# Kernel tuning notes

Measured on AMD Instinct MI355X. Metric: run time of the kernel, lower is better.

Reference implementation:

```python
import jax, jax.numpy as jnp
import numpy as np

EMBED_DIM = 1024
NUM_HEADS = 16
HEAD_DIM = EMBED_DIM // NUM_HEADS
ROPE_BASE = 10000.0


def _rope_angles(seq_len, head_dim):
    inv_freq = 1.0 / (ROPE_BASE ** (jnp.arange(0, head_dim, 2, dtype=jnp.float32) / head_dim))  # [D/2]
    pos = jnp.arange(seq_len, dtype=jnp.float32)
    ang = pos[:, None] * inv_freq[None, :]  # [S, D/2]
    return jnp.cos(ang), jnp.sin(ang)


def _apply_rope(t, cos, sin):
    # t: [B, H, S, D]; rotate-half convention
    d2 = t.shape[-1] // 2
    t1, t2 = t[..., :d2], t[..., d2:]
    return jnp.concatenate([t1 * cos - t2 * sin, t2 * cos + t1 * sin], axis=-1)


def setup_inputs() -> dict:
    key = jax.random.key(0)
    ks = jax.random.split(key, 6)
    B, S, E = 1, 4096, EMBED_DIM
    x = jax.random.normal(ks[0], (B, S, E), dtype=jnp.float32)
    # causal mask: True means masked-out (upper triangle above diagonal)
    mask = jnp.triu(jnp.ones((S, S), dtype=bool), k=1)[None, None, :, :]
    scale = 0.02
    wqkv_w = jax.random.normal(ks[1], (E, 3 * E), dtype=jnp.float32) * scale
    wqkv_b = jax.random.normal(ks[2], (3 * E,), dtype=jnp.float32) * scale
    out_w = jax.random.normal(ks[3], (E, E), dtype=jnp.float32) * scale
    out_b = jax.random.normal(ks[4], (E,), dtype=jnp.float32) * scale
    return {"x": x, "mask": mask, "wqkv_w": wqkv_w, "wqkv_b": wqkv_b, "out_w": out_w, "out_b": out_b}


def reference(x, mask, wqkv_w, wqkv_b, out_w, out_b):
    B, S, E = x.shape
    H, D = NUM_HEADS, HEAD_DIM
    qkv = x @ wqkv_w + wqkv_b  # [B, S, 3E]
    q, k, v = jnp.split(qkv, 3, axis=-1)
    # [B, S, E] -> [B, H, S, D]
    q = q.reshape(B, S, H, D).transpose(0, 2, 1, 3)
    k = k.reshape(B, S, H, D).transpose(0, 2, 1, 3)
    v = v.reshape(B, S, H, D).transpose(0, 2, 1, 3)
    cos, sin = _rope_angles(S, D)  # [S, D/2]
    q = _apply_rope(q, cos, sin)
    k = _apply_rope(k, cos, sin)
    scores = jnp.einsum('bhqd,bhkd->bhqk', q, k) * (D ** -0.5)  # [B, H, S, S]
    scores = jnp.where(mask[:, :, -S:, :], -jnp.inf, scores)
    weights = jax.nn.softmax(scores, axis=-1)
    ctx = jnp.einsum('bhqk,bhkd->bhqd', weights, v)  # [B, H, S, D]
    ctx = ctx.transpose(0, 2, 1, 3).reshape(B, S, E)
    return ctx @ out_w + out_b
```

## Files before the change

kernel.cpp:

```cpp
#include <hip/hip_runtime.h>
#include <hip/hip_bf16.h>
#include <math.h>

#define S_LEN 4096
#define EMB   1024
#define E3    3072
#define NH    16
#define HD    64

#define SLOTS_PER_HEAD 52
#define NSLOTS         832

typedef unsigned short u16;
typedef short          bfrag __attribute__((ext_vector_type(8)));
typedef float          ffrag __attribute__((ext_vector_type(4)));
typedef unsigned short us8   __attribute__((ext_vector_type(8)));
typedef unsigned short us4   __attribute__((ext_vector_type(4)));

__device__ __forceinline__ u16 f2bf(float f) {
    union { float f; unsigned u; } v; v.f = f;
    unsigned r = v.u + 0x7fffu + ((v.u >> 16) & 1u);
    return (u16)(r >> 16);
}
__device__ __forceinline__ float bf2f(u16 b) {
    union { unsigned u; float f; } v; v.u = ((unsigned)b) << 16;
    return v.f;
}
__device__ __forceinline__ unsigned pack_bf16_trunc(float lo, float hi) {
    union { float f; unsigned u; } a, b; a.f = lo; b.f = hi;
    return __builtin_amdgcn_perm(b.u, a.u, 0x07060302u);
}
__device__ __forceinline__ void gld16(const void* g, void* l) {
    __builtin_amdgcn_global_load_lds(
        (const __attribute__((address_space(1))) unsigned int*)g,
        (__attribute__((address_space(3))) unsigned int*)l, 16, 0, 0);
}

__global__ __launch_bounds__(256)
void cast_bf16_kernel(const float* __restrict__ in, u16* __restrict__ out) {
    const size_t i = ((size_t)blockIdx.x * 256 + threadIdx.x) * 8;
    float4 a = *(const float4*)(in + i);
    float4 b = *(const float4*)(in + i + 4);
    us8 o;
    o[0]=f2bf(a.x); o[1]=f2bf(a.y); o[2]=f2bf(a.z); o[3]=f2bf(a.w);
    o[4]=f2bf(b.x); o[5]=f2bf(b.y); o[6]=f2bf(b.z); o[7]=f2bf(b.w);
    *(us8*)(out + i) = o;
}

__global__ __launch_bounds__(256)
void transpose_cast_kernel(const float* __restrict__ in, u16* __restrict__ out,
                           int R, int C) {
    __shared__ u16 T[64][72];
    const int r0 = blockIdx.x * 64, c0 = blockIdx.y * 64;
    const int t = threadIdx.x;
    const int rr = t >> 2, cc = (t & 3) * 16;

    const float* ip = in + (size_t)(r0 + rr) * C + c0 + cc;
    u16 tmp[16];
    #pragma unroll
    for (int i4 = 0; i4 < 4; i4++) {
        float4 v = ((const float4*)ip)[i4];
        tmp[4*i4+0]=f2bf(v.x); tmp[4*i4+1]=f2bf(v.y);
        tmp[4*i4+2]=f2bf(v.z); tmp[4*i4+3]=f2bf(v.w);
    }
    #pragma unroll
    for (int i8 = 0; i8 < 2; i8++) {
        us8 vv;
        #pragma unroll
        for (int j = 0; j < 8; j++) vv[j] = tmp[8*i8+j];
        *(us8*)&T[rr][cc + 8*i8] = vv;
    }
    __syncthreads();

    const int oc = t >> 2, orr = (t & 3) * 16;
    u16 ot[16];
    #pragma unroll
    for (int j = 0; j < 16; j++) ot[j] = T[orr + j][oc];
    u16* op = out + (size_t)(c0 + oc) * R + r0 + orr;
    #pragma unroll
    for (int i8 = 0; i8 < 2; i8++) {
        us8 vv;
        #pragma unroll
        for (int j = 0; j < 8; j++) vv[j] = ot[8*i8+j];
        *(us8*)(op + 8*i8) = vv;
    }
}

template <int OUT_BF16, int NT, int ROPE, int MINW>
__global__ __launch_bounds__(256, MINW)
void gemm_bt_kernel(const u16* __restrict__ A, const u16* __restrict__ Bt,
                    const float* __restrict__ bias, void* __restrict__ Cv,
                    u16* __restrict__ vtp, int M, int N, int K) {
    constexpr int BN = 32 * NT;
    constexpr int WS = 16 * NT;
    __shared__ u16 As[2][128][32];
    __shared__ u16 Bs[2][BN][32];

    const int tid = threadIdx.x;
    const int w = tid >> 6, L = tid & 63;
    const int col = L & 15, quad = L >> 4;
    const int wm = w & 1, wn = w >> 1;
    const int m0 = blockIdx.x * 128, n0 = blockIdx.y * BN;

    ffrag acc[4][NT];
    #pragma unroll
    for (int a = 0; a < 4; a++)
        #pragma unroll
        for (int b = 0; b < NT; b++)
            #pragma unroll
            for (int r = 0; r < 4; r++) acc[a][b][r] = 0.f;

    const int srow = L >> 2;
    const int schk = L & 3;

    #pragma unroll
    for (int t = 0; t < 2; t++) {
        const int rg = (2 * w + t) * 16;
        gld16(A + (size_t)(m0 + rg + srow) * K + schk * 8, &As[0][rg][0]);
    }
    #pragma unroll
    for (int t = 0; t < NT / 2; t++) {
        const int rg = (w * (NT / 2) + t) * 16;
        gld16(Bt + (size_t)(n0 + rg + srow) * K + schk * 8, &Bs[0][rg][0]);
    }
    __syncthreads();

    int buf = 0;
    for (int k0 = 0; k0 < K; k0 += 32, buf ^= 1) {
        if (k0 + 32 < K) {
            #pragma unroll
            for (int t = 0; t < 2; t++) {
                const int rg = (2 * w + t) * 16;
                gld16(A + (size_t)(m0 + rg + srow) * K + k0 + 32 + schk * 8,
                      &As[buf ^ 1][rg][0]);
            }
            #pragma unroll
            for (int t = 0; t < NT / 2; t++) {
                const int rg = (w * (NT / 2) + t) * 16;
                gld16(Bt + (size_t)(n0 + rg + srow) * K + k0 + 32 + schk * 8,
                      &Bs[buf ^ 1][rg][0]);
            }
        }

        bfrag af[4], bf[NT];
        #pragma unroll
        for (int mt = 0; mt < 4; mt++)
            af[mt] = *(const bfrag*)&As[buf][64 * wm + 16 * mt + col][8 * quad];
        #pragma unroll
        for (int nt = 0; nt < NT; nt++)
            bf[nt] = *(const bfrag*)&Bs[buf][WS * wn + 16 * nt + col][8 * quad];
        #pragma unroll
        for (int mt = 0; mt < 4; mt++)
            #pragma unroll
            for (int nt = 0; nt < NT; nt++)
                acc[mt][nt] = __builtin_amdgcn_mfma_f32_16x16x32_bf16(
                    af[mt], bf[nt], acc[mt][nt], 0, 0, 0);

        __syncthreads();
    }

    float bv[NT];
    #pragma unroll
    for (int nt = 0; nt < NT; nt++) bv[nt] = bias[n0 + WS * wn + 16 * nt + col];

    if (ROPE && n0 < 2 * EMB) {
        const float SCq = (n0 < EMB) ? 0.125f * 1.44269504088896f : 1.0f;
        const float C = 13.287712379549449f / 32.0f;
        float invf[2];
        invf[0] = exp2f(-(float)col * C);
        invf[1] = exp2f(-(float)(col + 16) * C);
        #pragma unroll
        for (int mt = 0; mt < 4; mt++) {
            #pragma unroll
            for (int r = 0; r < 4; r++) {
                const int mrow = m0 + 64 * wm + 16 * mt + 4 * quad + r;
                const float fs = (float)mrow;
                u16* cp = (u16*)Cv + (size_t)mrow * N + n0 + 64 * wn + col;
                #pragma unroll
                for (int pr = 0; pr < 2; pr++) {
                    float sn, cs;
                    sincosf(fs * invf[pr], &sn, &cs);
                    const float t1 = acc[mt][pr][r] + bv[pr];
                    const float t2 = acc[mt][pr + 2][r] + bv[pr + 2];
                    cp[16 * pr]      = f2bf((t1 * cs - t2 * sn) * SCq);
                    cp[16 * pr + 32] = f2bf((t2 * cs + t1 * sn) * SCq);
                }
            }
        }
    } else if (ROPE) {
        #pragma unroll
        for (int nt = 0; nt < NT; nt++) {
            const int dg = n0 - 2 * EMB + WS * wn + 16 * nt + col;
            #pragma unroll
            for (int mt = 0; mt < 4; mt++) {
                const int s0 = m0 + 64 * wm + 16 * mt + 4 * quad;
                us4 pk;
                #pragma unroll
                for (int r = 0; r < 4; r++) pk[r] = f2bf(acc[mt][nt][r] + bv[nt]);
                *(us4*)&vtp[(size_t)dg * S_LEN + s0] = pk;
            }
        }
    } else {
        #pragma unroll
        for (int mt = 0; mt < 4; mt++) {
            #pragma unroll
            for (int r = 0; r < 4; r++) {
                const int m = m0 + 64 * wm + 16 * mt + 4 * quad + r;
                #pragma unroll
                for (int nt = 0; nt < NT; nt++) {
                    const int n = n0 + WS * wn + 16 * nt + col;
                    const float val = acc[mt][nt][r] + bv[nt];
                    if (OUT_BF16) ((u16*)Cv)[(size_t)m * N + n] = f2bf(val);
                    else          ((float*)Cv)[(size_t)m * N + n] = val;
                }
            }
        }
    }
}

__global__ __launch_bounds__(256, 3)
void flash10_kernel(const u16* __restrict__ qkvb, const u16* __restrict__ vt,
                    u16* __restrict__ ctxb, u16* __restrict__ pO,
                    float* __restrict__ pL) {
    __shared__ u16 QP[4][32][64];
    __shared__ u16 Ks[2][64][64];
    __shared__ u16 Vs[2][64][64];

    const int id = blockIdx.x;
    const int x  = id & 7;
    const int tt = id >> 3;
    const int h  = x + 8 * (tt & 1);
    const int o  = tt >> 1;

    int qi, ch, nc;
    if (o < 30)      { qi = 31 - o / 3;        ch = o % 3;        nc = 3; }
    else if (o < 33) { qi = 10 - (o - 30);     ch = 0;            nc = 1; }
    else if (o < 55) { const int oo = o - 33;  qi = 21 - oo / 2;  ch = oo & 1; nc = 2; }
    else             { qi = 7 - (o - 55);      ch = 0;            nc = 1; }

    const int total = 2 * qi + 2;
    const int Lc    = (total + nc - 1) / nc;
    const int kt0   = ch * Lc;
    const int cnt   = min(Lc, total - kt0);
    const bool lastch = (kt0 + cnt == total);
    const int q0 = qi * 128;

    const int tid = threadIdx.x;
    const int w = tid >> 6, L = tid & 63;
    const int col = L & 15, quad = L >> 4;
    const int lr = L >> 3, lp = L & 7;
    const int lc = lp ^ lr;

    const bool domask = lastch;
    const int nwt = cnt - ((domask && w < 2) ? 1 : 0);

    const size_t kArow = (size_t)(16 * w + lr) * E3 + EMB + h * HD + lc * 8;
    const size_t vArow = ((size_t)h * HD + 16 * w + lr) * S_LEN + lc * 8;
    const size_t kt0off  = (size_t)kt0 * 64 * E3;
    const size_t vt0off  = (size_t)kt0 * 64;

    #pragma unroll
    for (int u = 0; u < 4; u++)
        gld16(qkvb + (size_t)(q0 + 32 * w + 8 * u + lr) * E3 + h * HD + lc * 8,
              &QP[w][8 * u][0]);
    #pragma unroll
    for (int u = 0; u < 2; u++) {
        gld16(qkvb + kArow + kt0off + (size_t)(8 * u) * E3,
              &Ks[0][16 * w + 8 * u][0]);
        gld16(vt + vArow + vt0off + (size_t)(8 * u) * S_LEN,
              &Vs[0][16 * w + 8 * u][0]);
    }
    __syncthreads();

    bfrag qf[2][2];
    #pragma unroll
    for (int i = 0; i < 2; i++)
        #pragma unroll
        for (int ks = 0; ks < 2; ks++)
            qf[i][ks] = *(const bfrag*)
                ((const char*)&QP[w][16 * i + col][0] +
                 16 * ((4 * ks + quad) ^ (col & 7)));

    bfrag ones;
    #pragma unroll
    for (int i = 0; i < 8; i++) ones[i] = (short)0x3F80;

    ffrag o_[4][2], ol[2];
    #pragma unroll
    for (int d4 = 0; d4 < 4; d4++)
        #pragma unroll
        for (int i = 0; i < 2; i++)
            #pragma unroll
            for (int r2 = 0; r2 < 4; r2++) o_[d4][i][r2] = 0.f;
    #pragma unroll
    for (int i = 0; i < 2; i++)
        #pragma unroll
        for (int r2 = 0; r2 < 4; r2++) ol[i][r2] = 0.f;

    #pragma unroll 1
    for (int t = 0; t < cnt; t++) {
        const int buf = t & 1;
        if (t + 1 < cnt) {
            const size_t ko = kArow + kt0off + (size_t)(t + 1) * 64 * E3;
            const size_t vo = vArow + vt0off + (size_t)(t + 1) * 64;
            #pragma unroll
            for (int u = 0; u < 2; u++) {
                gld16(qkvb + ko + (size_t)(8 * u) * E3,
                      &Ks[buf ^ 1][16 * w + 8 * u][0]);
                gld16(vt + vo + (size_t)(8 * u) * S_LEN,
                      &Vs[buf ^ 1][16 * w + 8 * u][0]);
            }
        }

        if (t < nwt) {
            ffrag st[4][2];
            #pragma unroll
            for (int t4 = 0; t4 < 4; t4++)
                #pragma unroll
                for (int i = 0; i < 2; i++)
                    #pragma unroll
                    for (int r2 = 0; r2 < 4; r2++) st[t4][i][r2] = 0.f;
            #pragma unroll
            for (int ks = 0; ks < 2; ks++) {
                bfrag kf[4];
                #pragma unroll
                for (int t4 = 0; t4 < 4; t4++)
                    kf[t4] = *(const bfrag*)
                        &Ks[buf][16 * t4 + col][(((4 * ks + quad) ^ (col & 7)) * 8)];
                #pragma unroll
                for (int t4 = 0; t4 < 4; t4++)
                    #pragma unroll
                    for (int i = 0; i < 2; i++)
                        st[t4][i] = __builtin_amdgcn_mfma_f32_16x16x32_bf16(
                            kf[t4], qf[i][ks], st[t4][i], 0, 0, 0);
            }

            if (domask && t == nwt - 1) {
                #pragma unroll
                for (int i = 0; i < 2; i++) {
                    const int qrel = 32 * (w & 1) + 16 * i + col;
                    #pragma unroll
                    for (int t4 = 0; t4 < 4; t4++) {
                        const int key0 = 16 * t4 + 4 * quad;
                        #pragma unroll
                        for (int r2 = 0; r2 < 4; r2++)
                            if (key0 + r2 > qrel) st[t4][i][r2] = -3.0e38f;
                    }
                }
            }

            #pragma unroll
            for (int i = 0; i < 2; i++) {
                const int prow = 16 * i + col;
                #pragma unroll
                for (int t4 = 0; t4 < 4; t4++) {
                    float pr[4];
                    #pragma unroll
                    for (int r2 = 0; r2 < 4; r2++) pr[r2] = exp2f(st[t4][i][r2]);
                    uint2 pk;
                    pk.x = pack_bf16_trunc(pr[0], pr[1]);
                    pk.y = pack_bf16_trunc(pr[2], pr[3]);
                    const int c2 = (2 * t4 + (quad >> 1)) ^ (col & 7);
                    *(uint2*)((char*)&QP[w][prow][0] + 16 * c2 + 8 * (quad & 1)) = pk;
                }
            }

            #pragma unroll
            for (int ks = 0; ks < 2; ks++) {
                bfrag vf[4];
                #pragma unroll
                for (int d4 = 0; d4 < 4; d4++)
                    vf[d4] = *(const bfrag*)
                        &Vs[buf][16 * d4 + col][(((4 * ks + quad) ^ (col & 7)) * 8)];
                bfrag pf[2];
                #pragma unroll
                for (int i = 0; i < 2; i++)
                    pf[i] = *(const bfrag*)
                        ((const char*)&QP[w][16 * i + col][0] +
                         16 * ((4 * ks + quad) ^ (col & 7)));
                #pragma unroll
                for (int d4 = 0; d4 < 4; d4++)
                    #pragma unroll
                    for (int i = 0; i < 2; i++)
                        o_[d4][i] = __builtin_amdgcn_mfma_f32_16x16x32_bf16(
                            vf[d4], pf[i], o_[d4][i], 0, 0, 0);
                #pragma unroll
                for (int i = 0; i < 2; i++)
                    ol[i] = __builtin_amdgcn_mfma_f32_16x16x32_bf16(
                        ones, pf[i], ol[i], 0, 0, 0);
            }
        }

        __syncthreads();
    }

    if (nc == 1) {
        #pragma unroll
        for (int i = 0; i < 2; i++) {
            const float inv = 1.0f / ol[i][0];
            const int qg = q0 + 32 * w + 16 * i + col;
            #pragma unroll
            for (int d4 = 0; d4 < 4; d4++) {
                us4 pk;
                #pragma unroll
                for (int r2 = 0; r2 < 4; r2++) pk[r2] = f2bf(o_[d4][i][r2] * inv);
                *(us4*)&ctxb[(size_t)qg * EMB + h * HD + 16 * d4 + 4 * quad] = pk;
            }
        }
    } else {
        const int jj = (qi <= 21) ? (qi - 11) * 2 + ch : 22 + (qi - 22) * 3 + ch;
        const int slot = h * SLOTS_PER_HEAD + jj;
        u16* po = pO + (size_t)slot * (128 * 64);
        float* pl = pL + slot * 128;
        #pragma unroll
        for (int i = 0; i < 2; i++) {
            const int qrow = 32 * w + 16 * i + col;
            #pragma unroll
            for (int d4 = 0; d4 < 4; d4++) {
                us4 pk;
                #pragma unroll
                for (int r2 = 0; r2 < 4; r2++) pk[r2] = f2bf(o_[d4][i][r2]);
                *(us4*)&po[(size_t)qrow * 64 + 16 * d4 + 4 * quad] = pk;
            }
            if (quad == 0) pl[qrow] = ol[i][0];
        }
    }
}

__global__ __launch_bounds__(256)
void combine_kernel(const u16* __restrict__ pO, const float* __restrict__ pL,
                    u16* __restrict__ ctxb) {
    const int g = blockIdx.x;
    const int h = g / 21, qq = g % 21;
    const int qi = 11 + qq;
    const int nc = (qi <= 21) ? 2 : 3;
    const int jj0 = (qi <= 21) ? (qi - 11) * 2 : 22 + (qi - 22) * 3;
    const int slot0 = h * SLOTS_PER_HEAD + jj0;

    const int t = threadIdx.x;
    const int q = t >> 1, dh = (t & 1) * 32;

    float l = 0.f;
    for (int p = 0; p < nc; p++) l += pL[(slot0 + p) * 128 + q];
    const float inv = 1.0f / l;

    u16* op = ctxb + (size_t)(qi * 128 + q) * EMB + h * HD + dh;

    #pragma unroll
    for (int j = 0; j < 4; j++) {
        float s[8] = {0.f, 0.f, 0.f, 0.f, 0.f, 0.f, 0.f, 0.f};
        for (int p = 0; p < nc; p++) {
            const us8 va = *(const us8*)
                (pO + ((size_t)(slot0 + p) * 128 + q) * 64 + dh + 8 * j);
            #pragma unroll
            for (int e = 0; e < 8; e++) s[e] += bf2f(va[e]);
        }
        us8 vo;
        #pragma unroll
        for (int e = 0; e < 8; e++) vo[e] = f2bf(s[e] * inv);
        *(us8*)(op + 8 * j) = vo;
    }
}

extern "C" void kernel_launch(void* const* d_in, const int* in_sizes, int n_in,
                              void* d_out, int out_size, void* d_ws, size_t ws_size,
                              hipStream_t stream) {
    const float* x      = (const float*)d_in[0];
    const float* wqkv_w = (const float*)d_in[2];
    const float* wqkv_b = (const float*)d_in[3];
    const float* out_w  = (const float*)d_in[4];
    const float* out_b  = (const float*)d_in[5];
    float* out = (float*)d_out;

    u16* qkvb = (u16*)d_ws;
    u16* ctxb = qkvb + (size_t)S_LEN * E3;
    u16* xb   = ctxb + (size_t)S_LEN * EMB;
    u16* wt   = xb   + (size_t)S_LEN * EMB;
    u16* owt  = wt   + (size_t)E3 * EMB;
    u16* vtb  = owt  + (size_t)EMB * EMB;

    u16*   pO = xb;
    float* pL = (float*)(xb + (size_t)NSLOTS * 128 * 64);

    dim3 blk(256);

    cast_bf16_kernel<<<dim3(S_LEN * EMB / (256 * 8)), blk, 0, stream>>>(x, xb);
    transpose_cast_kernel<<<dim3(EMB / 64, E3 / 64), blk, 0, stream>>>(
        wqkv_w, wt, EMB, E3);
    transpose_cast_kernel<<<dim3(EMB / 64, EMB / 64), blk, 0, stream>>>(
        out_w, owt, EMB, EMB);

    gemm_bt_kernel<1, 4, 1, 3><<<dim3(S_LEN / 128, E3 / 128), blk, 0, stream>>>(
        xb, wt, wqkv_b, qkvb, vtb, S_LEN, E3, EMB);

    flash10_kernel<<<dim3(1008), blk, 0, stream>>>(qkvb, vtb, ctxb, pO, pL);
    combine_kernel<<<dim3(336), blk, 0, stream>>>(pO, pL, ctxb);

    gemm_bt_kernel<0, 2, 0, 2><<<dim3(S_LEN / 128, EMB / 64), blk, 0, stream>>>(
        ctxb, owt, out_b, out, nullptr, S_LEN, EMB, EMB);
}
```

Before: 249.4 us.

## Load V fragments directly from global and precompute RoPE sin/cos table

```diff
diff --git a/kernel.cpp b/kernel.cpp
--- a/kernel.cpp
+++ b/kernel.cpp
@@ -34,6 +34,17 @@
     __builtin_amdgcn_global_load_lds(
         (const __attribute__((address_space(1))) unsigned int*)g,
         (__attribute__((address_space(3))) unsigned int*)l, 16, 0, 0);
+}
+
+__global__ __launch_bounds__(256)
+void rope_tab_kernel(float2* __restrict__ tab) {
+    const int idx = blockIdx.x * 256 + threadIdx.x;
+    const int s = idx >> 5, j = idx & 31;
+    const float C = 13.287712379549449f / 32.0f;
+    const float invf = exp2f(-(float)j * C);
+    float sn, cs;
+    sincosf((float)s * invf, &sn, &cs);
+    tab[idx] = make_float2(cs, sn);
 }
 
 __global__ __launch_bounds__(256)
@@ -90,7 +101,8 @@
 __global__ __launch_bounds__(256, MINW)
 void gemm_bt_kernel(const u16* __restrict__ A, const u16* __restrict__ Bt,
                     const float* __restrict__ bias, void* __restrict__ Cv,
-                    u16* __restrict__ vtp, int M, int N, int K) {
+                    u16* __restrict__ vtp, const float2* __restrict__ rope,
+                    int M, int N, int K) {
     constexpr int BN = 32 * NT;
     constexpr int WS = 16 * NT;
     __shared__ u16 As[2][128][32];
@@ -165,21 +177,16 @@
 
     if (ROPE && n0 < 2 * EMB) {
         const float SCq = (n0 < EMB) ? 0.125f * 1.44269504088896f : 1.0f;
-        const float C = 13.287712379549449f / 32.0f;
-        float invf[2];
-        invf[0] = exp2f(-(float)col * C);
-        invf[1] = exp2f(-(float)(col + 16) * C);
         #pragma unroll
         for (int mt = 0; mt < 4; mt++) {
             #pragma unroll
             for (int r = 0; r < 4; r++) {
                 const int mrow = m0 + 64 * wm + 16 * mt + 4 * quad + r;
-                const float fs = (float)mrow;
                 u16* cp = (u16*)Cv + (size_t)mrow * N + n0 + 64 * wn + col;
                 #pragma unroll
                 for (int pr = 0; pr < 2; pr++) {
-                    float sn, cs;
-                    sincosf(fs * invf[pr], &sn, &cs);
+                    const float2 t = rope[(size_t)mrow * 32 + col + 16 * pr];
+                    const float cs = t.x, sn = t.y;
                     const float t1 = acc[mt][pr][r] + bv[pr];
                     const float t2 = acc[mt][pr + 2][r] + bv[pr + 2];
                     cp[16 * pr]      = f2bf((t1 * cs - t2 * sn) * SCq);
@@ -218,13 +225,12 @@
     }
 }
 
-__global__ __launch_bounds__(256, 3)
-void flash10_kernel(const u16* __restrict__ qkvb, const u16* __restrict__ vt,
+__global__ __launch_bounds__(256, 4)
+void flash11_kernel(const u16* __restrict__ qkvb, const u16* __restrict__ vt,
                     u16* __restrict__ ctxb, u16* __restrict__ pO,
                     float* __restrict__ pL) {
     __shared__ u16 QP[4][32][64];
     __shared__ u16 Ks[2][64][64];
-    __shared__ u16 Vs[2][64][64];
 
     const int id = blockIdx.x;
     const int x  = id & 7;
@@ -255,21 +261,18 @@
     const int nwt = cnt - ((domask && w < 2) ? 1 : 0);
 
     const size_t kArow = (size_t)(16 * w + lr) * E3 + EMB + h * HD + lc * 8;
-    const size_t vArow = ((size_t)h * HD + 16 * w + lr) * S_LEN + lc * 8;
     const size_t kt0off  = (size_t)kt0 * 64 * E3;
-    const size_t vt0off  = (size_t)kt0 * 64;
+    const u16* vbase = vt + (size_t)(h * HD + col) * S_LEN
+                          + (size_t)kt0 * 64 + 8 * quad;
 
     #pragma unroll
     for (int u = 0; u < 4; u++)
         gld16(qkvb + (size_t)(q0 + 32 * w + 8 * u + lr) * E3 + h * HD + lc * 8,
               &QP[w][8 * u][0]);
     #pragma unroll
-    for (int u = 0; u < 2; u++) {
+    for (int u = 0; u < 2; u++)
         gld16(qkvb + kArow + kt0off + (size_t)(8 * u) * E3,
               &Ks[0][16 * w + 8 * u][0]);
-        gld16(vt + vArow + vt0off + (size_t)(8 * u) * S_LEN,
-              &Vs[0][16 * w + 8 * u][0]);
-    }
     __syncthreads();
 
     bfrag qf[2][2];
@@ -300,16 +303,18 @@
     #pragma unroll 1
     for (int t = 0; t < cnt; t++) {
         const int buf = t & 1;
+
+        bfrag vA[4];
+        #pragma unroll
+        for (int d4 = 0; d4 < 4; d4++)
+            vA[d4] = *(const bfrag*)(vbase + (size_t)(16 * d4) * S_LEN + t * 64);
+
         if (t + 1 < cnt) {
             const size_t ko = kArow + kt0off + (size_t)(t + 1) * 64 * E3;
-            const size_t vo = vArow + vt0off + (size_t)(t + 1) * 64;
-            #pragma unroll
-            for (int u = 0; u < 2; u++) {
+            #pragma unroll
+            for (int u = 0; u < 2; u++)
                 gld16(qkvb + ko + (size_t)(8 * u) * E3,
                       &Ks[buf ^ 1][16 * w + 8 * u][0]);
-                gld16(vt + vo + (size_t)(8 * u) * S_LEN,
-                      &Vs[buf ^ 1][16 * w + 8 * u][0]);
-            }
         }
 
         if (t < nwt) {
@@ -334,6 +339,12 @@
                         st[t4][i] = __builtin_amdgcn_mfma_f32_16x16x32_bf16(
                             kf[t4], qf[i][ks], st[t4][i], 0, 0, 0);
             }
+
+            bfrag vB[4];
+            #pragma unroll
+            for (int d4 = 0; d4 < 4; d4++)
+                vB[d4] = *(const bfrag*)
+                    (vbase + (size_t)(16 * d4) * S_LEN + t * 64 + 32);
 
             if (domask && t == nwt - 1) {
                 #pragma unroll
@@ -367,11 +378,6 @@
 
             #pragma unroll
             for (int ks = 0; ks < 2; ks++) {
-                bfrag vf[4];
-                #pragma unroll
-                for (int d4 = 0; d4 < 4; d4++)
-                    vf[d4] = *(const bfrag*)
-                        &Vs[buf][16 * d4 + col][(((4 * ks + quad) ^ (col & 7)) * 8)];
                 bfrag pf[2];
                 #pragma unroll
                 for (int i = 0; i < 2; i++)
@@ -383,7 +389,7 @@
                     #pragma unroll
                     for (int i = 0; i < 2; i++)
                         o_[d4][i] = __builtin_amdgcn_mfma_f32_16x16x32_bf16(
-                            vf[d4], pf[i], o_[d4][i], 0, 0, 0);
+                            (ks ? vB : vA)[d4], pf[i], o_[d4][i], 0, 0, 0);
                 #pragma unroll
                 for (int i = 0; i < 2; i++)
                     ol[i] = __builtin_amdgcn_mfma_f32_16x16x32_bf16(
@@ -482,8 +488,11 @@
     u16*   pO = xb;
     float* pL = (float*)(xb + (size_t)NSLOTS * 128 * 64);
 
+    float2* ropetab = (float2*)ctxb;
+
     dim3 blk(256);
 
+    rope_tab_kernel<<<dim3(S_LEN * 32 / 256), blk, 0, stream>>>(ropetab);
     cast_bf16_kernel<<<dim3(S_LEN * EMB / (256 * 8)), blk, 0, stream>>>(x, xb);
     transpose_cast_kernel<<<dim3(EMB / 64, E3 / 64), blk, 0, stream>>>(
         wqkv_w, wt, EMB, E3);
@@ -491,11 +500,11 @@
         out_w, owt, EMB, EMB);
 
     gemm_bt_kernel<1, 4, 1, 3><<<dim3(S_LEN / 128, E3 / 128), blk, 0, stream>>>(
-        xb, wt, wqkv_b, qkvb, vtb, S_LEN, E3, EMB);
-
-    flash10_kernel<<<dim3(1008), blk, 0, stream>>>(qkvb, vtb, ctxb, pO, pL);
+        xb, wt, wqkv_b, qkvb, vtb, ropetab, S_LEN, E3, EMB);
+
+    flash11_kernel<<<dim3(1008), blk, 0, stream>>>(qkvb, vtb, ctxb, pO, pL);
     combine_kernel<<<dim3(336), blk, 0, stream>>>(pO, pL, ctxb);
 
     gemm_bt_kernel<0, 2, 0, 2><<<dim3(S_LEN / 128, EMB / 64), blk, 0, stream>>>(
-        ctxb, owt, out_b, out, nullptr, S_LEN, EMB, EMB);
-}
+        ctxb, owt, out_b, out, nullptr, nullptr, S_LEN, EMB, EMB);
+}
```

Measured after the change: 344.9 us. 1.38x slower.
